# Kernel tuning notes

Hardware: AMD Instinct MI355X
Metric: run time of the kernel (lower is better)

## Reference

```python
import jax, jax.numpy as jnp
import numpy as np

H, KVH, D = 8, 4, 256
SCALING = 256.0 ** -0.5   # query_pre_attn_scalar ** -0.5
SOFTCAP = 50.0
THETA = 10000.0
WINDOW = 1024


def setup_inputs() -> dict:
    key = jax.random.key(0)
    ks = jax.random.split(key, 5)
    B, S, HID = 2, 2048, 2304
    return {
        "hidden_states": jax.random.normal(ks[0], (B, S, HID), jnp.float32),
        "Wq": jax.random.normal(ks[1], (H * D, HID), jnp.float32) * 0.02,
        "Wk": jax.random.normal(ks[2], (KVH * D, HID), jnp.float32) * 0.02,
        "Wv": jax.random.normal(ks[3], (KVH * D, HID), jnp.float32) * 0.02,
        "Wo": jax.random.normal(ks[4], (HID, H * D), jnp.float32) * 0.02,
        "position_ids": jnp.arange(S, dtype=jnp.int32),
    }


def _rotate_half(x):
    x1, x2 = x[..., : D // 2], x[..., D // 2 :]
    return jnp.concatenate((-x2, x1), axis=-1)


def reference(hidden_states, Wq, Wk, Wv, Wo, position_ids):
    B, S, HID = hidden_states.shape
    # projections (torch Linear: y = x @ W.T)
    q = (hidden_states @ Wq.T).reshape(B, S, H, D).transpose(0, 2, 1, 3)      # [B,H,S,D]
    k = (hidden_states @ Wk.T).reshape(B, S, KVH, D).transpose(0, 2, 1, 3)    # [B,KVH,S,D]
    v = (hidden_states @ Wv.T).reshape(B, S, KVH, D).transpose(0, 2, 1, 3)

    # rotary embedding
    inv_freq = 1.0 / (THETA ** (jnp.arange(0, D, 2, dtype=jnp.float32) / D))  # [D/2]
    freqs = position_ids.astype(jnp.float32)[:, None] * inv_freq[None, :]     # [S,D/2]
    emb = jnp.concatenate((freqs, freqs), axis=-1)                            # [S,D]
    cos = jnp.cos(emb)[None, None]                                            # [1,1,S,D]
    sin = jnp.sin(emb)[None, None]
    q = q * cos + _rotate_half(q) * sin
    k = k * cos + _rotate_half(k) * sin

    # repeat_kv (GQA)
    n_rep = H // KVH
    k = jnp.repeat(k, n_rep, axis=1)  # [B,H,S,D]
    v = jnp.repeat(v, n_rep, axis=1)

    # softcapped attention scores
    scores = jnp.einsum("bhqd,bhkd->bhqk", q, k) * SCALING
    scores = SOFTCAP * jnp.tanh(scores / SOFTCAP)

    # causal + sliding-window mask
    i = jnp.arange(S)[:, None]
    j = jnp.arange(S)[None, :]
    allowed = (j <= i) & (i - j < WINDOW)
    scores = jnp.where(allowed[None, None], scores, jnp.finfo(scores.dtype).min)

    attn = jax.nn.softmax(scores.astype(jnp.float32), axis=-1).astype(q.dtype)
    out = jnp.einsum("bhqk,bhkd->bhqd", attn, v)          # [B,H,S,D]
    out = out.transpose(0, 2, 1, 3).reshape(B, S, H * D)   # [B,S,H*D]
    return out @ Wo.T                                      # [B,S,HID]
```

## Files before the change

### kernel.cpp

```cpp
#include <hip/hip_runtime.h>

typedef _Float16 half8 __attribute__((ext_vector_type(8)));
typedef _Float16 half4v __attribute__((ext_vector_type(4)));
typedef float floatx4 __attribute__((ext_vector_type(4)));

#define GLD16(g, l) __builtin_amdgcn_global_load_lds(                          \
    (__attribute__((address_space(1))) void*)(g),                              \
    (__attribute__((address_space(3))) void*)(l), 16, 0, 0)

#define VM0 asm volatile("s_waitcnt vmcnt(0)" ::: "memory")

__global__ void cvt_all(const float* __restrict__ s0, const float* __restrict__ s1,
                        const float* __restrict__ s2, const float* __restrict__ s3,
                        const float* __restrict__ s4, _Float16* __restrict__ d0,
                        _Float16* __restrict__ d1, _Float16* __restrict__ d2,
                        _Float16* __restrict__ d3, _Float16* __restrict__ d4) {
  long i = (long)blockIdx.x * 256 + threadIdx.x;
  const float* s;
  _Float16* d;
  long off;
  if (i < 2359296) { s = s0; d = d0; off = i; }
  else if (i < 3538944) { s = s1; d = d1; off = i - 2359296; }
  else if (i < 4128768) { s = s2; d = d2; off = i - 3538944; }
  else if (i < 4718592) { s = s3; d = d3; off = i - 4128768; }
  else { s = s4; d = d4; off = i - 4718592; }
  const float4 v = *(const float4*)(s + off * 4);
  half4v o = {(_Float16)v.x, (_Float16)v.y, (_Float16)v.z, (_Float16)v.w};
  *(half4v*)(d + off * 4) = o;
}

__device__ __forceinline__ void stg_half(const _Float16* __restrict__ g,
                                         _Float16* l, int h, long k0, int K,
                                         int tid, const long* gofs) {
#pragma unroll
  for (int p = 0; p < 2; ++p)
    GLD16(g + (long)h * 128 * K + k0 + gofs[p],
          l + (h * 1024 + p * 512 + tid) * 8);
}

#define BAR                                                                    \
  __builtin_amdgcn_sched_barrier(0);                                           \
  __builtin_amdgcn_s_barrier();                                                \
  __builtin_amdgcn_sched_barrier(0)

#define LDB(buf)                                                               \
  _Pragma("unroll") for (int n = 0; n < 4; ++n)                                \
  _Pragma("unroll") for (int ks = 0; ks < 2; ++ks)                             \
      bfr[n][ks] = *(const half8*)&lB[buf][boff0 + n * 1024 +                  \
                                           (((ks * 4 + quad) ^ xq) << 3)];

#define READA(DST, buf, q)                                                     \
  _Pragma("unroll") for (int m2 = 0; m2 < 2; ++m2)                             \
  _Pragma("unroll") for (int ks = 0; ks < 2; ++ks)                             \
      DST[m2][ks] = *(const half8*)&lA[buf][aoff0 + ((q) * 2 + m2) * 1024 +    \
                                            (((ks * 4 + quad) ^ xq) << 3)];

#define MFMA16(AF, q)                                                          \
  __builtin_amdgcn_s_setprio(1);                                               \
  _Pragma("unroll") for (int ks = 0; ks < 2; ++ks)                             \
  _Pragma("unroll") for (int m2 = 0; m2 < 2; ++m2)                             \
  _Pragma("unroll") for (int n = 0; n < 4; ++n)                                \
      acc[(q) * 2 + m2][n] = __builtin_amdgcn_mfma_f32_16x16x32_f16(           \
          AF[m2][ks], bfr[n][ks], acc[(q) * 2 + m2][n], 0, 0, 0);              \
  __builtin_amdgcn_s_setprio(0)

template <typename TO>
__global__ __launch_bounds__(512, 2) void gemm256(
    const _Float16* __restrict__ A, const _Float16* __restrict__ B,
    TO* __restrict__ C, int M, int N, int K) {
  __shared__ __align__(16) _Float16 lA[2][16384];
  __shared__ __align__(16) _Float16 lB[2][16384];
  const int tid = threadIdx.x;
  const int lane = tid & 63;
  const int w = tid >> 6;
  const int wm = w >> 2, wn = w & 3;
  const int quad = lane >> 4, l15 = lane & 15;
  const int xq = l15 & 7;

  const int nwg = gridDim.x * gridDim.y;
  int wg = blockIdx.y * gridDim.x + blockIdx.x;
  if (!(nwg & 7)) wg = (wg & 7) * (nwg >> 3) + (wg >> 3);
  const int bx = wg % gridDim.x, by = wg / gridDim.x;
  const long tM = (long)by * 256, tN = (long)bx * 256;

  const _Float16* Ab = A + tM * K;
  const _Float16* Bb = B + tN * K;

  long gofs[2];
#pragma unroll
  for (int p = 0; p < 2; ++p) {
    const int U = p * 512 + tid;
    const int r = U >> 3;
    gofs[p] = (long)r * K + (((U & 7) ^ (r & 7)) << 3);
  }

  const int aoff0 = (wm * 128 + l15) * 64;
  const int boff0 = (wn * 64 + l15) * 64;

  floatx4 acc[8][4] = {};
  half8 bfr[4][2];
  half8 afA[2][2], afB[2][2];

  stg_half(Ab, &lA[0][0], 0, 0, K, tid, gofs);
  stg_half(Ab, &lA[0][0], 1, 0, K, tid, gofs);
  stg_half(Bb, &lB[0][0], 0, 0, K, tid, gofs);
  stg_half(Bb, &lB[0][0], 1, 0, K, tid, gofs);
  VM0;
  BAR;
  LDB(0);
  READA(afA, 0, 0);

  const int NI = K >> 7;
  for (int i = 0; i < NI; ++i) {
    const long k1 = ((long)i << 7) + 64;
    const long k2 = k1 + 64;
    const bool fin = (i == NI - 1);
    BAR;
    stg_half(Ab, &lA[1][0], 0, k1, K, tid, gofs);
    stg_half(Ab, &lA[1][0], 1, k1, K, tid, gofs);
    stg_half(Bb, &lB[1][0], 0, k1, K, tid, gofs);
    stg_half(Bb, &lB[1][0], 1, k1, K, tid, gofs);
    READA(afB, 0, 1);
    MFMA16(afA, 0);
    BAR;
    READA(afA, 0, 2);
    MFMA16(afB, 1);
    BAR;
    READA(afB, 0, 3);
    MFMA16(afA, 2);
    VM0;
    BAR;
    MFMA16(afB, 3);
    LDB(1);
    READA(afA, 1, 0);
    BAR;
    if (!fin) {
      stg_half(Ab, &lA[0][0], 0, k2, K, tid, gofs);
      stg_half(Ab, &lA[0][0], 1, k2, K, tid, gofs);
      stg_half(Bb, &lB[0][0], 0, k2, K, tid, gofs);
      stg_half(Bb, &lB[0][0], 1, k2, K, tid, gofs);
    }
    READA(afB, 1, 1);
    MFMA16(afA, 0);
    BAR;
    READA(afA, 1, 2);
    MFMA16(afB, 1);
    BAR;
    READA(afB, 1, 3);
    MFMA16(afA, 2);
    if (!fin) VM0;
    BAR;
    MFMA16(afB, 3);
    if (!fin) {
      LDB(0);
      READA(afA, 0, 0);
    }
  }

#pragma unroll
  for (int m = 0; m < 8; ++m) {
#pragma unroll
    for (int n = 0; n < 4; ++n) {
      const long col = tN + wn * 64 + n * 16 + l15;
      const long row0 = tM + wm * 128 + m * 16 + quad * 4;
#pragma unroll
      for (int r = 0; r < 4; ++r)
        C[(row0 + r) * N + col] = (TO)acc[m][n][r];
    }
  }
}

__global__ void rope_qk(const _Float16* __restrict__ QKV,
                        const int* __restrict__ pos_ids,
                        _Float16* __restrict__ Qr, _Float16* __restrict__ Kr) {
  const int idx = blockIdx.x * blockDim.x + threadIdx.x;
  const int d = idx & 127;
  const int rest = idx >> 7;
  const int head = rest % 12;
  const int ms = rest / 12;
  const int s = ms & 2047;
  const int b = ms >> 11;
  const float ang = (float)pos_ids[s] * __expf(d * -0.07195578164f);
  const float c = __cosf(ang), sn = __sinf(ang);
  if (head < 8) {
    const _Float16* src = QKV + (long)ms * 4096 + head * 256 + d;
    const float x1 = (float)src[0], x2 = (float)src[128];
    _Float16* dst = Qr + (((long)b * 8 + head) * 2048 + s) * 256 + d;
    dst[0] = (_Float16)(x1 * c - x2 * sn);
    dst[128] = (_Float16)(x2 * c + x1 * sn);
  } else {
    const int kh = head - 8;
    const _Float16* src = QKV + (long)ms * 4096 + 2048 + kh * 256 + d;
    const float x1 = (float)src[0], x2 = (float)src[128];
    _Float16* dst = Kr + (((long)b * 4 + kh) * 2048 + s) * 256 + d;
    dst[0] = (_Float16)(x1 * c - x2 * sn);
    dst[128] = (_Float16)(x2 * c + x1 * sn);
  }
}

__global__ void vtrans(const _Float16* __restrict__ QKV,
                       _Float16* __restrict__ Vt) {
  __shared__ _Float16 lT[64 * 65];
  const int tid = threadIdx.x;
  const int ss = blockIdx.x * 64;
  const int dd = blockIdx.y * 64;
  const int z = blockIdx.z;
  const int b = z >> 2, kvh = z & 3;

#pragma unroll
  for (int pass = 0; pass < 2; ++pass) {
    const int U = pass * 256 + tid;
    const int s_loc = U >> 3, du = U & 7;
    const half8 v = *(const half8*)(QKV + ((long)(b * 2048 + ss + s_loc)) * 4096 +
                                    3072 + kvh * 256 + dd + du * 8);
#pragma unroll
    for (int e = 0; e < 8; ++e) lT[s_loc * 65 + du * 8 + e] = v[e];
  }
  __syncthreads();
#pragma unroll
  for (int pass = 0; pass < 2; ++pass) {
    const int U = pass * 256 + tid;
    const int su = U & 7, dl = (U >> 3) & 63;
    half8 o;
#pragma unroll
    for (int e = 0; e < 8; ++e) o[e] = lT[(su * 8 + e) * 65 + dl];
    *(half8*)(Vt + ((long)z * 256 + dd + dl) * 2048 + ss + su * 8) = o;
  }
}

__global__ __launch_bounds__(256, 2) void attn_fwd(
    const _Float16* __restrict__ Q, const _Float16* __restrict__ K,
    const _Float16* __restrict__ Vt, _Float16* __restrict__ AO) {
  __shared__ __align__(16) _Float16 lK[2][64 * 256];
  __shared__ __align__(16) _Float16 lP[64 * 76];

  const int tid = threadIdx.x;
  const int lane = tid & 63;
  const int w = tid >> 6;
  const int quad = lane >> 4, l15 = lane & 15;

  const int qt = blockIdx.x;
  const int h = blockIdx.y;
  const int b = blockIdx.z;
  const int kvh = h >> 1;
  const int qs = qt * 64;

  const _Float16* Qb = Q + (((long)b * 8 + h) * 2048) * 256;
  const _Float16* Kb = K + (((long)b * 4 + kvh) * 2048) * 256;
  const _Float16* Vb = Vt + (((long)b * 4 + kvh) * 256) * 2048;

  half8 qf[8];
  {
    const _Float16* qp = Qb + (long)(qs + w * 16 + l15) * 256 + quad * 8;
#pragma unroll
    for (int t = 0; t < 8; ++t) qf[t] = *(const half8*)(qp + t * 32);
  }
  half8 onesv;
#pragma unroll
  for (int e = 0; e < 8; ++e) onesv[e] = (_Float16)1.f;

  floatx4 o[4][4] = {};
  floatx4 lacc[4] = {};

  const int kt_lo = qt >= 16 ? qt - 16 : 0;

  {
    const _Float16* kt0 = Kb + (long)kt_lo * 64 * 256;
#pragma unroll
    for (int p = 0; p < 8; ++p) {
      const int U = p * 256 + tid;
      const int r = U >> 5, u = U & 31;
      GLD16(kt0 + r * 256 + ((u ^ (r & 7)) << 3), &lK[0][U * 8]);
    }
  }

  int cur = 0;
  for (int kt = kt_lo; kt <= qt; ++kt, cur ^= 1) {
    const int ks = kt * 64;
    __syncthreads();

    half8 vf[2][4];
#pragma unroll
    for (int t2 = 0; t2 < 2; ++t2)
#pragma unroll
      for (int j = 0; j < 4; ++j) {
        const int d = w * 64 + j * 16 + l15;
        vf[t2][j] = *(const half8*)(Vb + (long)d * 2048 + ks + t2 * 32 + quad * 8);
      }
    if (kt < qt) {
      const _Float16* kt0 = Kb + (long)(ks + 64) * 256;
      const int nxt = cur ^ 1;
#pragma unroll
      for (int p = 0; p < 8; ++p) {
        const int U = p * 256 + tid;
        const int r = U >> 5, u = U & 31;
        GLD16(kt0 + r * 256 + ((u ^ (r & 7)) << 3), &lK[nxt][U * 8]);
      }
    }

    floatx4 sc[4] = {};
#pragma unroll
    for (int t = 0; t < 8; ++t)
#pragma unroll
      for (int j = 0; j < 4; ++j) {
        const half8 kf = *(const half8*)&lK[cur][(j * 16 + l15) * 256 +
                                                 (((t * 4 + quad) ^ (l15 & 7)) << 3)];
        sc[j] = __builtin_amdgcn_mfma_f32_16x16x32_f16(qf[t], kf, sc[j], 0, 0, 0);
      }

    const bool need_mask = (kt == qt) || (kt == qt - 16);
    const int qr0 = qs + w * 16 + quad * 4;
#pragma unroll
    for (int j = 0; j < 4; ++j) {
      const int key = ks + j * 16 + l15;
#pragma unroll
      for (int r = 0; r < 4; ++r) {
        const float s = sc[j][r] * 0.0625f;
        const float t2 = (s * 0.02f) * (s * 0.02f);
        const float cap = s * (1.f + t2 * (-0.33333333f + t2 * 0.13333333f));
        float p = __expf(cap - 5.f);
        if (need_mask) {
          const bool ok = (key <= qr0 + r) && (qr0 + r - key < 1024);
          p = ok ? p : 0.f;
        }
        lP[(w * 16 + quad * 4 + r) * 76 + j * 16 + l15] = (_Float16)p;
      }
    }
    __syncthreads();

#pragma unroll
    for (int t2 = 0; t2 < 2; ++t2) {
      half8 pf[4];
#pragma unroll
      for (int i = 0; i < 4; ++i)
        pf[i] = *(const half8*)&lP[(i * 16 + l15) * 76 + t2 * 32 + quad * 8];
#pragma unroll
      for (int i = 0; i < 4; ++i) {
        lacc[i] = __builtin_amdgcn_mfma_f32_16x16x32_f16(pf[i], onesv, lacc[i],
                                                         0, 0, 0);
#pragma unroll
        for (int j = 0; j < 4; ++j)
          o[i][j] = __builtin_amdgcn_mfma_f32_16x16x32_f16(pf[i], vf[t2][j],
                                                           o[i][j], 0, 0, 0);
      }
    }
  }

  _Float16* aop = AO + ((long)b * 2048 + qs) * 2048 + (long)h * 256;
#pragma unroll
  for (int i = 0; i < 4; ++i)
#pragma unroll
    for (int r = 0; r < 4; ++r) {
      const int row = i * 16 + quad * 4 + r;
      const float inv = 1.0f / lacc[i][r];
#pragma unroll
      for (int j = 0; j < 4; ++j)
        aop[(long)row * 2048 + w * 64 + j * 16 + l15] =
            (_Float16)(o[i][j][r] * inv);
    }
}

extern "C" void kernel_launch(void* const* d_in, const int* in_sizes, int n_in,
                              void* d_out, int out_size, void* d_ws,
                              size_t ws_size, hipStream_t stream) {
  const float* hs = (const float*)d_in[0];
  const float* Wq = (const float*)d_in[1];
  const float* Wk = (const float*)d_in[2];
  const float* Wv = (const float*)d_in[3];
  const float* Wo = (const float*)d_in[4];
  const int* pos = (const int*)d_in[5];
  float* out = (float*)d_out;

  _Float16* Xf = (_Float16*)d_ws;
  _Float16* Wqkv = Xf + 4096L * 2304;
  _Float16* Wo16 = Wqkv + 4096L * 2304;
  _Float16* QKV = Wo16 + 2304L * 2048;
  _Float16* Qr = QKV + 4096L * 4096;
  _Float16* Kr = Qr + 2L * 8 * 2048 * 256;
  _Float16* Vt = Kr + 2L * 4 * 2048 * 256;
  _Float16* AO = Xf;

  cvt_all<<<dim3(23040), dim3(256), 0, stream>>>(
      hs, Wq, Wk, Wv, Wo, Xf, Wqkv, Wqkv + 2048L * 2304, Wqkv + 3072L * 2304,
      Wo16);

  gemm256<_Float16><<<dim3(16, 16), dim3(512), 0, stream>>>(Xf, Wqkv, QKV,
                                                            4096, 4096, 2304);
  rope_qk<<<dim3(2 * 2048 * 12 * 128 / 256), dim3(256), 0, stream>>>(QKV, pos,
                                                                     Qr, Kr);
  vtrans<<<dim3(32, 4, 8), dim3(256), 0, stream>>>(QKV, Vt);
  attn_fwd<<<dim3(32, 8, 2), dim3(256), 0, stream>>>(Qr, Kr, Vt, AO);
  gemm256<float><<<dim3(9, 16), dim3(512), 0, stream>>>(AO, Wo16, out, 4096,
                                                        2304, 2048);
}
```

Baseline: 361.8 us.

## Restructure GEMM main loop into finer-grained interleaved load/compute pipeline with transposed epilogue

Rewrites the 256x256 GEMM main loop so global-to-LDS staging of A and B halves is spread across the compute phases, using partial vmcnt/lgkmcnt waits instead of full drains. B fragments are double-buffered in registers (even/odd), LDS offsets are precomputed, and the last iteration is peeled. The epilogue now goes through a per-wave LDS transpose so each lane writes contiguous 16-element row segments with vector stores instead of scattered scalar stores. This adds register pressure from the extra fragment buffers and more barriers, and the partial waits carry a correctness risk.

```diff
diff --git a/kernel.cpp b/kernel.cpp
--- a/kernel.cpp
+++ b/kernel.cpp
@@ -8,7 +8,8 @@
     (__attribute__((address_space(1))) void*)(g),                              \
     (__attribute__((address_space(3))) void*)(l), 16, 0, 0)
 
-#define VM0 asm volatile("s_waitcnt vmcnt(0)" ::: "memory")
+#define VMC(N) asm volatile("s_waitcnt vmcnt(" #N ")" ::: "memory")
+#define LGK(N) asm volatile("s_waitcnt lgkmcnt(" #N ")" ::: "memory")
 
 __global__ void cvt_all(const float* __restrict__ s0, const float* __restrict__ s1,
                         const float* __restrict__ s2, const float* __restrict__ s3,
@@ -43,26 +44,32 @@
   __builtin_amdgcn_s_barrier();                                                \
   __builtin_amdgcn_sched_barrier(0)
 
-#define LDB(buf)                                                               \
-  _Pragma("unroll") for (int n = 0; n < 4; ++n)                                \
-  _Pragma("unroll") for (int ks = 0; ks < 2; ++ks)                             \
-      bfr[n][ks] = *(const half8*)&lB[buf][boff0 + n * 1024 +                  \
-                                           (((ks * 4 + quad) ^ xq) << 3)];
-
-#define READA(DST, buf, q)                                                     \
-  _Pragma("unroll") for (int m2 = 0; m2 < 2; ++m2)                             \
-  _Pragma("unroll") for (int ks = 0; ks < 2; ++ks)                             \
-      DST[m2][ks] = *(const half8*)&lA[buf][aoff0 + ((q) * 2 + m2) * 1024 +    \
-                                            (((ks * 4 + quad) ^ xq) << 3)];
-
-#define MFMA16(AF, q)                                                          \
-  __builtin_amdgcn_s_setprio(1);                                               \
-  _Pragma("unroll") for (int ks = 0; ks < 2; ++ks)                             \
-  _Pragma("unroll") for (int m2 = 0; m2 < 2; ++m2)                             \
-  _Pragma("unroll") for (int n = 0; n < 4; ++n)                                \
-      acc[(q) * 2 + m2][n] = __builtin_amdgcn_mfma_f32_16x16x32_f16(           \
-          AF[m2][ks], bfr[n][ks], acc[(q) * 2 + m2][n], 0, 0, 0);              \
-  __builtin_amdgcn_s_setprio(0)
+#define RDA(DST, buf, q)                                                       \
+  do {                                                                         \
+    DST[0][0] = *(const half8*)&lA[buf][ah0 + ((q) * 2 + 0) * 1024];           \
+    DST[0][1] = *(const half8*)&lA[buf][ah1 + ((q) * 2 + 0) * 1024];           \
+    DST[1][0] = *(const half8*)&lA[buf][ah0 + ((q) * 2 + 1) * 1024];           \
+    DST[1][1] = *(const half8*)&lA[buf][ah1 + ((q) * 2 + 1) * 1024];           \
+  } while (0)
+
+#define RDB(DST, buf)                                                          \
+  do {                                                                         \
+    _Pragma("unroll") for (int n = 0; n < 4; ++n) {                            \
+      DST[n][0] = *(const half8*)&lB[buf][bh0 + n * 1024];                     \
+      DST[n][1] = *(const half8*)&lB[buf][bh1 + n * 1024];                     \
+    }                                                                          \
+  } while (0)
+
+#define MM(AF, BF, q)                                                          \
+  do {                                                                         \
+    __builtin_amdgcn_s_setprio(1);                                             \
+    _Pragma("unroll") for (int ks = 0; ks < 2; ++ks)                           \
+    _Pragma("unroll") for (int m2 = 0; m2 < 2; ++m2)                           \
+    _Pragma("unroll") for (int n = 0; n < 4; ++n)                              \
+        acc[(q) * 2 + m2][n] = __builtin_amdgcn_mfma_f32_16x16x32_f16(         \
+            AF[m2][ks], BF[n][ks], acc[(q) * 2 + m2][n], 0, 0, 0);             \
+    __builtin_amdgcn_s_setprio(0);                                             \
+  } while (0)
 
 template <typename TO>
 __global__ __launch_bounds__(512, 2) void gemm256(
@@ -94,78 +101,148 @@
     gofs[p] = (long)r * K + (((U & 7) ^ (r & 7)) << 3);
   }
 
-  const int aoff0 = (wm * 128 + l15) * 64;
-  const int boff0 = (wn * 64 + l15) * 64;
+  const int ah0 = (wm * 128 + l15) * 64 + (((0 * 4 + quad) ^ xq) << 3);
+  const int ah1 = (wm * 128 + l15) * 64 + (((1 * 4 + quad) ^ xq) << 3);
+  const int bh0 = (wn * 64 + l15) * 64 + (((0 * 4 + quad) ^ xq) << 3);
+  const int bh1 = (wn * 64 + l15) * 64 + (((1 * 4 + quad) ^ xq) << 3);
 
   floatx4 acc[8][4] = {};
-  half8 bfr[4][2];
-  half8 afA[2][2], afB[2][2];
+  half8 afE[2][2], afO[2][2];
+  half8 bfrE[4][2], bfrO[4][2];
 
   stg_half(Ab, &lA[0][0], 0, 0, K, tid, gofs);
   stg_half(Ab, &lA[0][0], 1, 0, K, tid, gofs);
   stg_half(Bb, &lB[0][0], 0, 0, K, tid, gofs);
   stg_half(Bb, &lB[0][0], 1, 0, K, tid, gofs);
-  VM0;
+  stg_half(Bb, &lB[1][0], 0, 64, K, tid, gofs);
+  stg_half(Bb, &lB[1][0], 1, 64, K, tid, gofs);
+  VMC(4);
   BAR;
-  LDB(0);
-  READA(afA, 0, 0);
+  RDB(bfrE, 0);
 
   const int NI = K >> 7;
-  for (int i = 0; i < NI; ++i) {
+  for (int i = 0; i < NI - 1; ++i) {
     const long k1 = ((long)i << 7) + 64;
     const long k2 = k1 + 64;
-    const bool fin = (i == NI - 1);
-    BAR;
+    const long k3 = k2 + 64;
     stg_half(Ab, &lA[1][0], 0, k1, K, tid, gofs);
+    RDA(afE, 0, 0);
+    RDA(afO, 0, 1);
+    LGK(4);
+    BAR;
+    MM(afE, bfrE, 0);
+    BAR;
     stg_half(Ab, &lA[1][0], 1, k1, K, tid, gofs);
-    stg_half(Bb, &lB[1][0], 0, k1, K, tid, gofs);
-    stg_half(Bb, &lB[1][0], 1, k1, K, tid, gofs);
-    READA(afB, 0, 1);
-    MFMA16(afA, 0);
-    BAR;
-    READA(afA, 0, 2);
-    MFMA16(afB, 1);
-    BAR;
-    READA(afB, 0, 3);
-    MFMA16(afA, 2);
-    VM0;
-    BAR;
-    MFMA16(afB, 3);
-    LDB(1);
-    READA(afA, 1, 0);
-    BAR;
-    if (!fin) {
-      stg_half(Ab, &lA[0][0], 0, k2, K, tid, gofs);
-      stg_half(Ab, &lA[0][0], 1, k2, K, tid, gofs);
-      stg_half(Bb, &lB[0][0], 0, k2, K, tid, gofs);
-      stg_half(Bb, &lB[0][0], 1, k2, K, tid, gofs);
-    }
-    READA(afB, 1, 1);
-    MFMA16(afA, 0);
-    BAR;
-    READA(afA, 1, 2);
-    MFMA16(afB, 1);
-    BAR;
-    READA(afB, 1, 3);
-    MFMA16(afA, 2);
-    if (!fin) VM0;
-    BAR;
-    MFMA16(afB, 3);
-    if (!fin) {
-      LDB(0);
-      READA(afA, 0, 0);
-    }
-  }
-
+    RDA(afE, 0, 2);
+    BAR;
+    MM(afO, bfrE, 1);
+    BAR;
+    stg_half(Bb, &lB[0][0], 0, k2, K, tid, gofs);
+    RDA(afO, 0, 3);
+    BAR;
+    MM(afE, bfrE, 2);
+    VMC(6);
+    BAR;
+    stg_half(Bb, &lB[0][0], 1, k2, K, tid, gofs);
+    RDB(bfrO, 1);
+    BAR;
+    MM(afO, bfrE, 3);
+    VMC(4);
+    BAR;
+    stg_half(Ab, &lA[0][0], 0, k2, K, tid, gofs);
+    RDA(afE, 1, 0);
+    RDA(afO, 1, 1);
+    LGK(4);
+    BAR;
+    MM(afE, bfrO, 0);
+    BAR;
+    stg_half(Ab, &lA[0][0], 1, k2, K, tid, gofs);
+    RDA(afE, 1, 2);
+    BAR;
+    MM(afO, bfrO, 1);
+    BAR;
+    stg_half(Bb, &lB[1][0], 0, k3, K, tid, gofs);
+    RDA(afO, 1, 3);
+    BAR;
+    MM(afE, bfrO, 2);
+    VMC(6);
+    BAR;
+    stg_half(Bb, &lB[1][0], 1, k3, K, tid, gofs);
+    RDB(bfrE, 0);
+    BAR;
+    MM(afO, bfrO, 3);
+    VMC(4);
+    BAR;
+  }
+  {
+    const long k1 = ((long)(NI - 1) << 7) + 64;
+    stg_half(Ab, &lA[1][0], 0, k1, K, tid, gofs);
+    RDA(afE, 0, 0);
+    RDA(afO, 0, 1);
+    LGK(4);
+    BAR;
+    MM(afE, bfrE, 0);
+    BAR;
+    stg_half(Ab, &lA[1][0], 1, k1, K, tid, gofs);
+    RDA(afE, 0, 2);
+    BAR;
+    MM(afO, bfrE, 1);
+    BAR;
+    RDA(afO, 0, 3);
+    BAR;
+    MM(afE, bfrE, 2);
+    VMC(4);
+    BAR;
+    RDB(bfrO, 1);
+    BAR;
+    MM(afO, bfrE, 3);
+    VMC(0);
+    BAR;
+    RDA(afE, 1, 0);
+    RDA(afO, 1, 1);
+    LGK(4);
+    BAR;
+    MM(afE, bfrO, 0);
+    BAR;
+    RDA(afE, 1, 2);
+    BAR;
+    MM(afO, bfrO, 1);
+    BAR;
+    RDA(afO, 1, 3);
+    BAR;
+    MM(afE, bfrO, 2);
+    BAR;
+    MM(afO, bfrO, 3);
+    BAR;
+  }
+
+  float* lT = (float*)&lA[0][0] + (long)w * 1280;
+  const int erow = lane >> 2, ecb = lane & 3;
 #pragma unroll
   for (int m = 0; m < 8; ++m) {
 #pragma unroll
-    for (int n = 0; n < 4; ++n) {
-      const long col = tN + wn * 64 + n * 16 + l15;
-      const long row0 = tM + wm * 128 + m * 16 + quad * 4;
-#pragma unroll
-      for (int r = 0; r < 4; ++r)
-        C[(row0 + r) * N + col] = (TO)acc[m][n][r];
+    for (int n = 0; n < 4; ++n)
+      *(floatx4*)&lT[(n * 16 + l15) * 20 + quad * 4] = acc[m][n];
+    float v[16];
+#pragma unroll
+    for (int c = 0; c < 16; ++c) v[c] = lT[(ecb * 16 + c) * 20 + erow];
+    const long grow = tM + wm * 128 + m * 16 + erow;
+    TO* dst = C + grow * N + tN + wn * 64 + ecb * 16;
+    if constexpr (sizeof(TO) == 2) {
+      half8 o0, o1;
+#pragma unroll
+      for (int e = 0; e < 8; ++e) {
+        o0[e] = (_Float16)v[e];
+        o1[e] = (_Float16)v[8 + e];
+      }
+      *(half8*)(dst) = o0;
+      *(half8*)(dst + 8) = o1;
+    } else {
+#pragma unroll
+      for (int k4 = 0; k4 < 4; ++k4) {
+        float4 o = {v[k4 * 4], v[k4 * 4 + 1], v[k4 * 4 + 2], v[k4 * 4 + 3]};
+        *(float4*)(dst + k4 * 4) = o;
+      }
     }
   }
 }
```

Result: slower. 378.4 us (+4.6%).
